# Optimization experiments

Hardware: AMD Instinct MI355X
Metric: run time of the kernel (lower is better)

The kernel has to match this reference:

```python
import jax, jax.numpy as jnp
import numpy as np

K = 10          # hardcoded in module (self.K = 10)
H = 26          # neighbors per query point in this run
PAD_H = 28      # layer_ind2neighbor[layer_ind=0]
KP_EXTENT = 1.2 # linear-influence extent


def setup_inputs() -> dict:
    key = jax.random.key(0)
    ks = jax.random.split(key, 6)
    N, Ns, Cin, Cout = 65536, 65536, 64, 128
    q_pts = jax.random.normal(ks[0], (N, 3), jnp.float32)
    s_pts = jax.random.normal(ks[1], (Ns, 3), jnp.float32)
    neighb_inds = jax.random.randint(ks[2], (N, H), 0, Ns)
    x = jax.random.normal(ks[3], (Ns, Cin), jnp.float32)
    # kernel_points_generator: Linear(PAD_H*3 -> K*3)
    gen_W = jax.random.normal(ks[4], (K * 3, PAD_H * 3), jnp.float32) * (1.0 / np.sqrt(PAD_H * 3))
    gen_b = jnp.zeros((K * 3,), jnp.float32)
    # KPConv weights: [K, in, out] (kaiming_uniform in torch; scaled normal here)
    weights = jax.random.normal(ks[5], (K, Cin, Cout), jnp.float32) * (1.0 / np.sqrt(Cin))
    return {"q_pts": q_pts, "s_pts": s_pts, "x": x,
            "gen_W": gen_W, "gen_b": gen_b, "weights": weights,
            "neighb_inds": neighb_inds}


def _kpconv(q_pts, s_pts, x, gen_W, gen_b, weights, neighb_inds):
    N = q_pts.shape[0]
    # shadow support point far away (index Ns)
    s_pad = jnp.concatenate([s_pts, jnp.full((1, 3), 1e6, s_pts.dtype)], axis=0)
    neighbors = s_pad[neighb_inds] - q_pts[:, None, :]                          # [N,H,3]
    # generative kernel points: pad neighbor list with -1 up to PAD_H, run linear
    padded = jnp.concatenate(
        [neighbors, jnp.full((N, PAD_H - H, 3), -1.0, neighbors.dtype)], axis=1)
    kp = (padded.reshape(N, -1) @ gen_W.T + gen_b).reshape(N, 1, K, 3)          # [N,1,K,3]
    diff = neighbors[:, :, None, :] - kp                                        # [N,H,K,3]
    sq_d = jnp.sum(diff * diff, axis=3)                                         # [N,H,K]
    # KP_influence == 'linear'
    all_w = jnp.maximum(1.0 - jnp.sqrt(sq_d) / KP_EXTENT, 0.0)
    all_w = jnp.swapaxes(all_w, 1, 2)                                           # [N,K,H]
    # shadow feature row (zeros) at index Ns
    x_pad = jnp.concatenate([x, jnp.zeros((1, x.shape[1]), x.dtype)], axis=0)
    neighb_x = x_pad[neighb_inds]                                               # [N,H,Cin]
    weighted = jnp.einsum('nkh,nhi->nki', all_w, neighb_x)                      # [N,K,Cin]
    return jnp.einsum('nki,kio->no', weighted, weights)                         # [N,Cout]


def reference(q_pts, s_pts, x, gen_W, gen_b, weights, neighb_inds):
    return _kpconv(q_pts, s_pts, x, gen_W, gen_b, weights, neighb_inds)
```

## Files before the change

### kernel.cpp

```cpp
#include <hip/hip_runtime.h>
#include <stdint.h>

#define N_Q   65536
#define N_S   65536
#define NB_H  26
#define PAD_H 28
#define KP    10
#define CIN   64
#define COUT  128
#define MT    8
#define BM    64

typedef unsigned short u16x4  __attribute__((ext_vector_type(4)));
typedef unsigned short u16x8  __attribute__((ext_vector_type(8)));
typedef float          f32x4  __attribute__((ext_vector_type(4)));
typedef _Float16       f16x8  __attribute__((ext_vector_type(8)));
typedef _Float16       f16x2  __attribute__((ext_vector_type(2)));

#define CVT_BLOCKS 2049
#define PACK_BLOCKS 40

static __device__ __forceinline__ unsigned short f2h(float f) {
  return __builtin_bit_cast(unsigned short, (_Float16)f);
}

static __device__ __forceinline__ unsigned int pkrtz_u32(float a, float b) {
  return __builtin_bit_cast(unsigned int, __builtin_amdgcn_cvt_pkrtz(a, b));
}

static __device__ __forceinline__ float fdot2u(unsigned int a, unsigned int b, float c) {
#if __has_builtin(__builtin_amdgcn_fdot2)
  return __builtin_amdgcn_fdot2(__builtin_bit_cast(f16x2, a),
                                __builtin_bit_cast(f16x2, b), c, false);
#else
  f16x2 ha = __builtin_bit_cast(f16x2, a), hb = __builtin_bit_cast(f16x2, b);
  return c + (float)ha[0] * (float)hb[0] + (float)ha[1] * (float)hb[1];
#endif
}

__global__ void prep_kernel(const float* __restrict__ x,
                            const float* __restrict__ w,
                            unsigned short* __restrict__ xh,
                            unsigned short* __restrict__ bp) {
  if (blockIdx.x < CVT_BLOCKS) {
    long t = (long)blockIdx.x * blockDim.x + threadIdx.x;
    long off = t * 8;
    if (off >= (long)(N_S + 1) * CIN) return;
    u16x8 o;
    if (off < (long)N_S * CIN) {
      f32x4 a = *(const f32x4*)(x + off);
      f32x4 b = *(const f32x4*)(x + off + 4);
      o[0] = f2h(a[0]); o[1] = f2h(a[1]); o[2] = f2h(a[2]); o[3] = f2h(a[3]);
      o[4] = f2h(b[0]); o[5] = f2h(b[1]); o[6] = f2h(b[2]); o[7] = f2h(b[3]);
    } else {
      o = (u16x8)0;
    }
    *(u16x8*)(xh + off) = o;
  } else {
    int t = (blockIdx.x - CVT_BLOCKS) * blockDim.x + threadIdx.x;
    if (t >= 8 * 20 * 64) return;
    int lane = t & 63;
    int frag = t >> 6;
    int ks = frag % 20;
    int ct = frag / 20;
    int row0 = ks * 32 + (lane >> 4) * 8;
    int col  = ct * 16 + (lane & 15);
    u16x8 o;
    #pragma unroll
    for (int j = 0; j < 8; ++j) o[j] = f2h(w[(row0 + j) * COUT + col]);
    *(u16x8*)(bp + (long)t * 8) = o;
  }
}

__global__ void __launch_bounds__(256, 6)
kpconv_gather(const float* __restrict__ q_pts, const float* __restrict__ s_pts,
              const float* __restrict__ gen_W, const float* __restrict__ gen_b,
              const int* __restrict__ inds, const unsigned short* __restrict__ xh,
              unsigned short* __restrict__ wg) {

  __shared__ int          sh_ind[MT][NB_H];
  __shared__ float        sh_nbr[MT][80];
  __shared__ float        sh_kp[MT][KP * 3];
  __shared__ unsigned int sh_aw[MT][13][12];

  const int tid  = threadIdx.x;
  const int base = blockIdx.x * MT;

  if (tid < MT * NB_H) {
    int m = tid / NB_H, h = tid % NB_H;
    int n = base + m;
    int ind = inds[n * NB_H + h];
    sh_ind[m][h] = ind;
    float sx, sy, sz;
    if ((unsigned)ind < (unsigned)N_S) {
      sx = s_pts[ind * 3 + 0]; sy = s_pts[ind * 3 + 1]; sz = s_pts[ind * 3 + 2];
    } else {
      sx = 1e6f; sy = 1e6f; sz = 1e6f;
    }
    sh_nbr[m][h * 3 + 0] = sx - q_pts[n * 3 + 0];
    sh_nbr[m][h * 3 + 1] = sy - q_pts[n * 3 + 1];
    sh_nbr[m][h * 3 + 2] = sz - q_pts[n * 3 + 2];
  }
  if (tid < MT * 2) sh_nbr[tid >> 1][78 + (tid & 1)] = -1.0f;
  __syncthreads();

  if (tid < MT * KP * 3) {
    int m = tid / 30, r = tid % 30;
    const float* Wr = gen_W + r * (PAD_H * 3);
    const f32x4* W4 = (const f32x4*)Wr;
    const f32x4* N4 = (const f32x4*)&sh_nbr[m][0];
    f32x4 accv = {0.f, 0.f, 0.f, 0.f};
    #pragma unroll
    for (int j = 0; j < 20; ++j) accv += W4[j] * N4[j];
    sh_kp[m][r] = gen_b[r] - (Wr[80] + Wr[81] + Wr[82] + Wr[83])
                + accv[0] + accv[1] + accv[2] + accv[3];
  }
  __syncthreads();

  for (int p = tid; p < MT * 13 * KP; p += 256) {
    int k = p % KP;
    int t = p / KP;
    int m = t & (MT - 1);
    int hp = t >> 3;
    float kx = sh_kp[m][k * 3 + 0], ky = sh_kp[m][k * 3 + 1], kz = sh_kp[m][k * 3 + 2];
    int h0 = hp * 2;
    float dx0 = sh_nbr[m][h0 * 3 + 0] - kx;
    float dy0 = sh_nbr[m][h0 * 3 + 1] - ky;
    float dz0 = sh_nbr[m][h0 * 3 + 2] - kz;
    float w0 = fmaxf(1.0f - sqrtf(dx0 * dx0 + dy0 * dy0 + dz0 * dz0) * (1.0f / 1.2f), 0.0f);
    float dx1 = sh_nbr[m][h0 * 3 + 3] - kx;
    float dy1 = sh_nbr[m][h0 * 3 + 4] - ky;
    float dz1 = sh_nbr[m][h0 * 3 + 5] - kz;
    float w1 = fmaxf(1.0f - sqrtf(dx1 * dx1 + dy1 * dy1 + dz1 * dz1) * (1.0f / 1.2f), 0.0f);
    sh_aw[m][hp][k] = pkrtz_u32(w0, w1);
  }
  __syncthreads();

  {
    const int m  = tid >> 5;
    const int i0 = (tid & 31) * 2;
    float acc0[KP], acc1[KP];
    #pragma unroll
    for (int k = 0; k < KP; ++k) { acc0[k] = 0.f; acc1[k] = 0.f; }

    unsigned int xr[4];
    #pragma unroll
    for (int h = 0; h < 4; ++h)
      xr[h] = *(const unsigned int*)(xh + (long)sh_ind[m][h] * CIN + i0);

    #pragma unroll
    for (int p = 0; p < 13; ++p) {
      unsigned int r0 = xr[(2 * p) & 3];
      unsigned int r1 = xr[(2 * p + 1) & 3];
      if (2 * p + 4 < NB_H)
        xr[(2 * p) & 3] = *(const unsigned int*)(xh + (long)sh_ind[m][2 * p + 4] * CIN + i0);
      if (2 * p + 5 < NB_H)
        xr[(2 * p + 1) & 3] = *(const unsigned int*)(xh + (long)sh_ind[m][2 * p + 5] * CIN + i0);
      unsigned int pair0 = __builtin_amdgcn_perm(r1, r0, 0x05040100u);
      unsigned int pair1 = __builtin_amdgcn_perm(r1, r0, 0x07060302u);
      const unsigned int* wrow = &sh_aw[m][p][0];
      #pragma unroll
      for (int k = 0; k < KP; ++k) {
        unsigned int w2 = wrow[k];
        acc0[k] = fdot2u(w2, pair0, acc0[k]);
        acc1[k] = fdot2u(w2, pair1, acc1[k]);
      }
    }
    #pragma unroll
    for (int k = 0; k < KP; ++k) {
      __builtin_nontemporal_store(
          pkrtz_u32(acc0[k], acc1[k]),
          (unsigned int*)(wg + (long)(base + m) * (KP * CIN) + k * CIN + i0));
    }
  }
}

__global__ void __launch_bounds__(256, 4)
kpconv_gemm(const unsigned short* __restrict__ wg,
            const unsigned short* __restrict__ bp,
            float* __restrict__ out) {

  __shared__ unsigned short sA[2][BM][72];

  const int tid  = threadIdx.x;
  const int wave = tid >> 6;
  const int lane = tid & 63;
  const long row0 = (long)blockIdx.x * BM;

  const int srow = tid >> 3;
  const int scb  = tid & 7;

  {
    u16x8 a = __builtin_nontemporal_load((const u16x8*)(wg + (row0 + srow) * 640 + scb * 8));
    u16x8 b = __builtin_nontemporal_load((const u16x8*)(wg + (row0 + srow + 32) * 640 + scb * 8));
    *(u16x8*)&sA[0][srow][scb * 8] = a;
    *(u16x8*)&sA[0][srow + 32][scb * 8] = b;
  }

  f32x4 acc[4][2];
  #pragma unroll
  for (int rt = 0; rt < 4; ++rt)
    #pragma unroll
    for (int c = 0; c < 2; ++c) acc[rt][c] = (f32x4){0.f, 0.f, 0.f, 0.f};

  const int ct0  = wave * 2, ct1 = ct0 + 1;
  const int arow = lane & 15;
  const int aq   = lane >> 4;
  int cur = 0;

  for (int kc = 0; kc < 10; ++kc) {
    __syncthreads();
    u16x8 p0, p1;
    if (kc < 9) {
      p0 = __builtin_nontemporal_load((const u16x8*)(wg + (row0 + srow) * 640 + (kc + 1) * 64 + scb * 8));
      p1 = __builtin_nontemporal_load((const u16x8*)(wg + (row0 + srow + 32) * 640 + (kc + 1) * 64 + scb * 8));
    }
    #pragma unroll
    for (int ks2 = 0; ks2 < 2; ++ks2) {
      int ks = kc * 2 + ks2;
      u16x8 b0u = *(const u16x8*)(bp + (long)((ct0 * 20 + ks) * 64 + lane) * 8);
      u16x8 b1u = *(const u16x8*)(bp + (long)((ct1 * 20 + ks) * 64 + lane) * 8);
      f16x8 b0 = __builtin_bit_cast(f16x8, b0u);
      f16x8 b1 = __builtin_bit_cast(f16x8, b1u);
      #pragma unroll
      for (int rt = 0; rt < 4; ++rt) {
        u16x8 au = *(const u16x8*)&sA[cur][rt * 16 + arow][ks2 * 32 + aq * 8];
        f16x8 a = __builtin_bit_cast(f16x8, au);
        acc[rt][0] = __builtin_amdgcn_mfma_f32_16x16x32_f16(a, b0, acc[rt][0], 0, 0, 0);
        acc[rt][1] = __builtin_amdgcn_mfma_f32_16x16x32_f16(a, b1, acc[rt][1], 0, 0, 0);
      }
    }
    if (kc < 9) {
      *(u16x8*)&sA[1 - cur][srow][scb * 8] = p0;
      *(u16x8*)&sA[1 - cur][srow + 32][scb * 8] = p1;
      cur ^= 1;
    }
  }

  const int col   = lane & 15;
  const int rbase = aq * 4;
  #pragma unroll
  for (int rt = 0; rt < 4; ++rt)
    #pragma unroll
    for (int r = 0; r < 4; ++r) {
      long row = row0 + rt * 16 + rbase + r;
      __builtin_nontemporal_store(acc[rt][0][r], &out[row * COUT + ct0 * 16 + col]);
      __builtin_nontemporal_store(acc[rt][1][r], &out[row * COUT + ct1 * 16 + col]);
    }
}

extern "C" void kernel_launch(void* const* d_in, const int* in_sizes, int n_in,
                              void* d_out, int out_size, void* d_ws, size_t ws_size,
                              hipStream_t stream) {
  const float* q_pts = (const float*)d_in[0];
  const float* s_pts = (const float*)d_in[1];
  const float* x     = (const float*)d_in[2];
  const float* gen_W = (const float*)d_in[3];
  const float* gen_b = (const float*)d_in[4];
  const float* wts   = (const float*)d_in[5];
  const int*   inds  = (const int*)d_in[6];
  float* out = (float*)d_out;

  unsigned short* xh = (unsigned short*)d_ws;
  unsigned short* bp = xh + (size_t)(N_S + 1) * CIN;
  unsigned short* wg = bp + (size_t)81920;

  prep_kernel<<<CVT_BLOCKS + PACK_BLOCKS, 256, 0, stream>>>(x, wts, xh, bp);
  kpconv_gather<<<N_Q / MT, 256, 0, stream>>>(q_pts, s_pts, gen_W, gen_b,
                                              inds, xh, wg);
  kpconv_gemm<<<N_Q / BM, 256, 0, stream>>>(wg, bp, out);
}
```

Before: 174.3 us.

## Compact neighbors with nonzero kernel influence before gathering features

Each neighbor's ten linear-influence weights are now computed by one thread, and only neighbors with at least one positive weight are appended to a compacted per-point list through a shared atomic counter. The feature gather and accumulation then loop only over that list with packed fp32 FMAs, replacing the fp16 dot2 pairs, so loads and math for neighbors with zero influence are skipped. Launch-bounds occupancy is also raised from 6 to 8. This adds a data-dependent loop and atomic ordering, which can reorder the accumulation and add divergence. The gain depends on how sparse the weights are for the input distribution.

```diff
diff --git a/kernel.cpp b/kernel.cpp
--- a/kernel.cpp
+++ b/kernel.cpp
@@ -14,6 +14,7 @@
 typedef unsigned short u16x4  __attribute__((ext_vector_type(4)));
 typedef unsigned short u16x8  __attribute__((ext_vector_type(8)));
 typedef float          f32x4  __attribute__((ext_vector_type(4)));
+typedef float          f32x2  __attribute__((ext_vector_type(2)));
 typedef _Float16       f16x8  __attribute__((ext_vector_type(8)));
 typedef _Float16       f16x2  __attribute__((ext_vector_type(2)));
 
@@ -27,15 +28,11 @@
 static __device__ __forceinline__ unsigned int pkrtz_u32(float a, float b) {
   return __builtin_bit_cast(unsigned int, __builtin_amdgcn_cvt_pkrtz(a, b));
 }
-
-static __device__ __forceinline__ float fdot2u(unsigned int a, unsigned int b, float c) {
-#if __has_builtin(__builtin_amdgcn_fdot2)
-  return __builtin_amdgcn_fdot2(__builtin_bit_cast(f16x2, a),
-                                __builtin_bit_cast(f16x2, b), c, false);
-#else
-  f16x2 ha = __builtin_bit_cast(f16x2, a), hb = __builtin_bit_cast(f16x2, b);
-  return c + (float)ha[0] * (float)hb[0] + (float)ha[1] * (float)hb[1];
-#endif
+static __device__ __forceinline__ float h2f_lo(unsigned int u) {
+  return (float)__builtin_bit_cast(_Float16, (unsigned short)(u & 0xffffu));
+}
+static __device__ __forceinline__ float h2f_hi(unsigned int u) {
+  return (float)__builtin_bit_cast(_Float16, (unsigned short)(u >> 16));
 }
 
 __global__ void prep_kernel(const float* __restrict__ x,
@@ -72,7 +69,7 @@
   }
 }
 
-__global__ void __launch_bounds__(256, 6)
+__global__ void __launch_bounds__(256, 8)
 kpconv_gather(const float* __restrict__ q_pts, const float* __restrict__ s_pts,
               const float* __restrict__ gen_W, const float* __restrict__ gen_b,
               const int* __restrict__ inds, const unsigned short* __restrict__ xh,
@@ -81,11 +78,14 @@
   __shared__ int          sh_ind[MT][NB_H];
   __shared__ float        sh_nbr[MT][80];
   __shared__ float        sh_kp[MT][KP * 3];
-  __shared__ unsigned int sh_aw[MT][13][12];
+  __shared__ int          sh_cnt[MT];
+  __shared__ unsigned int sh_hoff[MT][NB_H];
+  __shared__ float        sh_w[MT][NB_H][12];
 
   const int tid  = threadIdx.x;
   const int base = blockIdx.x * MT;
 
+  if (tid < MT) sh_cnt[tid] = 0;
   if (tid < MT * NB_H) {
     int m = tid / NB_H, h = tid % NB_H;
     int n = base + m;
@@ -117,59 +117,78 @@
   }
   __syncthreads();
 
-  for (int p = tid; p < MT * 13 * KP; p += 256) {
-    int k = p % KP;
-    int t = p / KP;
-    int m = t & (MT - 1);
-    int hp = t >> 3;
-    float kx = sh_kp[m][k * 3 + 0], ky = sh_kp[m][k * 3 + 1], kz = sh_kp[m][k * 3 + 2];
-    int h0 = hp * 2;
-    float dx0 = sh_nbr[m][h0 * 3 + 0] - kx;
-    float dy0 = sh_nbr[m][h0 * 3 + 1] - ky;
-    float dz0 = sh_nbr[m][h0 * 3 + 2] - kz;
-    float w0 = fmaxf(1.0f - sqrtf(dx0 * dx0 + dy0 * dy0 + dz0 * dz0) * (1.0f / 1.2f), 0.0f);
-    float dx1 = sh_nbr[m][h0 * 3 + 3] - kx;
-    float dy1 = sh_nbr[m][h0 * 3 + 4] - ky;
-    float dz1 = sh_nbr[m][h0 * 3 + 5] - kz;
-    float w1 = fmaxf(1.0f - sqrtf(dx1 * dx1 + dy1 * dy1 + dz1 * dz1) * (1.0f / 1.2f), 0.0f);
-    sh_aw[m][hp][k] = pkrtz_u32(w0, w1);
+  if (tid < MT * NB_H) {
+    int m = tid / NB_H, h = tid % NB_H;
+    float nx = sh_nbr[m][h * 3 + 0];
+    float ny = sh_nbr[m][h * 3 + 1];
+    float nz = sh_nbr[m][h * 3 + 2];
+    float wv[KP];
+    bool any = false;
+    #pragma unroll
+    for (int k = 0; k < KP; ++k) {
+      float dx = nx - sh_kp[m][k * 3 + 0];
+      float dy = ny - sh_kp[m][k * 3 + 1];
+      float dz = nz - sh_kp[m][k * 3 + 2];
+      float d  = sqrtf(dx * dx + dy * dy + dz * dz);
+      float w  = fmaxf(1.0f - d * (1.0f / 1.2f), 0.0f);
+      wv[k] = w;
+      any = any || (w > 0.0f);
+    }
+    if (any) {
+      int s = atomicAdd(&sh_cnt[m], 1);
+      sh_hoff[m][s] = (unsigned int)sh_ind[m][h] * CIN;
+      #pragma unroll
+      for (int k = 0; k < KP; ++k) sh_w[m][s][k] = wv[k];
+    }
   }
   __syncthreads();
 
   {
     const int m  = tid >> 5;
     const int i0 = (tid & 31) * 2;
-    float acc0[KP], acc1[KP];
-    #pragma unroll
-    for (int k = 0; k < KP; ++k) { acc0[k] = 0.f; acc1[k] = 0.f; }
-
-    unsigned int xr[4];
-    #pragma unroll
-    for (int h = 0; h < 4; ++h)
-      xr[h] = *(const unsigned int*)(xh + (long)sh_ind[m][h] * CIN + i0);
-
-    #pragma unroll
-    for (int p = 0; p < 13; ++p) {
-      unsigned int r0 = xr[(2 * p) & 3];
-      unsigned int r1 = xr[(2 * p + 1) & 3];
-      if (2 * p + 4 < NB_H)
-        xr[(2 * p) & 3] = *(const unsigned int*)(xh + (long)sh_ind[m][2 * p + 4] * CIN + i0);
-      if (2 * p + 5 < NB_H)
-        xr[(2 * p + 1) & 3] = *(const unsigned int*)(xh + (long)sh_ind[m][2 * p + 5] * CIN + i0);
-      unsigned int pair0 = __builtin_amdgcn_perm(r1, r0, 0x05040100u);
-      unsigned int pair1 = __builtin_amdgcn_perm(r1, r0, 0x07060302u);
-      const unsigned int* wrow = &sh_aw[m][p][0];
-      #pragma unroll
-      for (int k = 0; k < KP; ++k) {
-        unsigned int w2 = wrow[k];
-        acc0[k] = fdot2u(w2, pair0, acc0[k]);
-        acc1[k] = fdot2u(w2, pair1, acc1[k]);
+    const int c  = sh_cnt[m];
+    f32x2 acc[KP];
+    #pragma unroll
+    for (int k = 0; k < KP; ++k) acc[k] = (f32x2){0.f, 0.f};
+
+    unsigned int xr0 = 0, xr1 = 0, xr2 = 0, xr3 = 0;
+    if (0 < c) xr0 = *(const unsigned int*)(xh + sh_hoff[m][0] + i0);
+    if (1 < c) xr1 = *(const unsigned int*)(xh + sh_hoff[m][1] + i0);
+    if (2 < c) xr2 = *(const unsigned int*)(xh + sh_hoff[m][2] + i0);
+    if (3 < c) xr3 = *(const unsigned int*)(xh + sh_hoff[m][3] + i0);
+
+    #define C_BODY(J, XR)                                                     \
+      {                                                                       \
+        unsigned int cur = XR;                                                \
+        if ((J) + 4 < c) XR = *(const unsigned int*)(xh + sh_hoff[m][(J) + 4] + i0); \
+        f32x2 xp = { h2f_lo(cur), h2f_hi(cur) };                              \
+        f32x4 wa = *(const f32x4*)&sh_w[m][J][0];                             \
+        f32x4 wb = *(const f32x4*)&sh_w[m][J][4];                             \
+        f32x2 wc = *(const f32x2*)&sh_w[m][J][8];                             \
+        acc[0] += (f32x2){wa[0], wa[0]} * xp;                                 \
+        acc[1] += (f32x2){wa[1], wa[1]} * xp;                                 \
+        acc[2] += (f32x2){wa[2], wa[2]} * xp;                                 \
+        acc[3] += (f32x2){wa[3], wa[3]} * xp;                                 \
+        acc[4] += (f32x2){wb[0], wb[0]} * xp;                                 \
+        acc[5] += (f32x2){wb[1], wb[1]} * xp;                                 \
+        acc[6] += (f32x2){wb[2], wb[2]} * xp;                                 \
+        acc[7] += (f32x2){wb[3], wb[3]} * xp;                                 \
+        acc[8] += (f32x2){wc[0], wc[0]} * xp;                                 \
+        acc[9] += (f32x2){wc[1], wc[1]} * xp;                                 \
       }
-    }
+
+    for (int j0 = 0; j0 < c; j0 += 4) {
+      C_BODY(j0, xr0);
+      if (j0 + 1 < c) C_BODY(j0 + 1, xr1);
+      if (j0 + 2 < c) C_BODY(j0 + 2, xr2);
+      if (j0 + 3 < c) C_BODY(j0 + 3, xr3);
+    }
+    #undef C_BODY
+
     #pragma unroll
     for (int k = 0; k < KP; ++k) {
       __builtin_nontemporal_store(
-          pkrtz_u32(acc0[k], acc1[k]),
+          pkrtz_u32(acc[k][0], acc[k][1]),
           (unsigned int*)(wg + (long)(base + m) * (KP * CIN) + k * CIN + i0));
     }
   }
```

New measurement: 176.8 us. Within noise of the previous version (+1.4%).
